# Optimization experiments

Hardware: AMD Instinct MI355X
Metric: run time of the kernel (lower is better)

Reference implementation:

```python
import jax, jax.numpy as jnp
import numpy as np

B, S_ENC, S_DEC, ENC_H, DEC_H = 8, 2048, 2048, 512, 512


def setup_inputs() -> dict:
    key = jax.random.key(0)
    k1, k2, k3 = jax.random.split(key, 3)
    return {
        "enc_hidden_states": jax.random.normal(k1, (B, S_ENC, ENC_H), dtype=jnp.float32),
        "dec_hidden_states": jax.random.normal(k2, (B, S_DEC, DEC_H), dtype=jnp.float32),
        "W_att": jax.random.normal(k3, (ENC_H, DEC_H), dtype=jnp.float32),
    }


def reference(enc_hidden_states, dec_hidden_states, W_att):
    # Project encoder states: [B, S_enc, dec_h]
    enc_proj = jnp.einsum("bse,ed->bsd", enc_hidden_states, W_att)
    # Luong 'general' scores for all decoder timesteps at once: [B, S_dec, S_enc]
    # (original code loops over decoder timesteps via tf.map_fn; this is the
    # equivalent single batched matmul)
    att_logits = jnp.einsum("btd,bsd->bts", dec_hidden_states, enc_proj)
    att_softmax = jax.nn.softmax(att_logits, axis=-1)
    # Attention context vectors: [B, S_dec, enc_h]
    att_vector = jnp.einsum("bts,bse->bte", att_softmax, enc_hidden_states)
    return att_vector
```

## Files before the change

kernel.cpp:

```cpp
#include <hip/hip_runtime.h>
#include <cstdint>


#define DEVINL __device__ __forceinline__

typedef __attribute__((ext_vector_type(8))) short short8;
typedef __attribute__((ext_vector_type(4))) float f32x4;

DEVINL short f2bf(float x) {
    union { float f; uint32_t u; } v; v.f = x;
    uint32_t r = v.u + 0x7FFFu + ((v.u >> 16) & 1u);
    return (short)(r >> 16);
}
DEVINL float bf2f(short h) {
    union { uint32_t u; float f; } v; v.u = ((uint32_t)(uint16_t)h) << 16;
    return v.f;
}

DEVINL void gload_lds16(const void* g, void* l) {
    __builtin_amdgcn_global_load_lds(
        (const __attribute__((address_space(1))) char*)g,
        (__attribute__((address_space(3))) char*)l, 16, 0, 0);
}

__global__ __launch_bounds__(256)
void split_kernel(const float* __restrict__ x, short* __restrict__ hi,
                  short* __restrict__ lo)
{
    long i = ((long)blockIdx.x * 256 + threadIdx.x) * 8;
    f32x4 a = *(const f32x4*)(x + i);
    f32x4 b = *(const f32x4*)(x + i + 4);
    short8 h, l;
#pragma unroll
    for (int j = 0; j < 4; j++) {
        short ha = f2bf(a[j]); h[j] = ha;     l[j] = f2bf(a[j] - bf2f(ha));
        short hb = f2bf(b[j]); h[4 + j] = hb; l[4 + j] = f2bf(b[j] - bf2f(hb));
    }
    *(short8*)(hi + i) = h;
    *(short8*)(lo + i) = l;
}

__global__ __launch_bounds__(256)
void split_w_kernel(const float* __restrict__ w, short* __restrict__ wth,
                    short* __restrict__ wtl)
{
    int idx = blockIdx.x * 256 + threadIdx.x;
    int k = idx >> 9, n = idx & 511;
    float v = w[idx];
    short h = f2bf(v);
    wth[(long)n * 512 + k] = h;
    wtl[(long)n * 512 + k] = f2bf(v - bf2f(h));
}

__global__ __launch_bounds__(256)
void transpose_bf16_kernel(const float* __restrict__ x, short* __restrict__ xt)
{
    __shared__ short tile[32][33];
    const int b  = blockIdx.z;
    const int s0 = blockIdx.x * 32;
    const int e0 = blockIdx.y * 32;
    const float* px = x + (long)b * 2048 * 512;
    short* pt = xt + (long)b * 512 * 2048;
    const int tx = threadIdx.x & 31;
    const int ty = threadIdx.x >> 5;
#pragma unroll
    for (int r = 0; r < 32; r += 8)
        tile[ty + r][tx] = f2bf(px[(long)(s0 + ty + r) * 512 + e0 + tx]);
    __syncthreads();
#pragma unroll
    for (int r = 0; r < 32; r += 8)
        pt[(long)(e0 + ty + r) * 2048 + s0 + tx] = tile[tx][ty + r];
}

template<int NTERMS, bool SPLIT_OUT>
__global__ __launch_bounds__(256, 2)
void gemm_bt(const short* __restrict__ Ah, const short* __restrict__ Al,
             const short* __restrict__ Bh, const short* __restrict__ Bl,
             float* __restrict__ C, short* __restrict__ Ch, short* __restrict__ Cl,
             int K, int lda, int ldb, int ldc,
             long sA, long sB, long sC)
{
    extern __shared__ char smem_raw[];
    constexpr int OPS = (NTERMS == 3) ? 4 : 2;
    constexpr int SET = 128 * 32 * OPS;
    short* smem = (short*)smem_raw;

    const int tid  = threadIdx.x;
    const int wave = tid >> 6;
    const int lane = tid & 63;
    const int quad = lane >> 4;
    const int l16  = lane & 15;
    const int wm   = (wave >> 1) * 64;
    const int wn   = (wave & 1) * 64;

    const long tile_m = (long)blockIdx.y * 128;
    const long tile_n = (long)blockIdx.x * 128;
    const int  bz     = blockIdx.z;

    const short* pAh = Ah + (long)bz * sA;
    const short* pBh = Bh + (long)bz * sB;
    const short* pAl = (NTERMS == 3) ? (Al + (long)bz * sA) : nullptr;
    const short* pBl = (NTERMS == 3) ? (Bl + (long)bz * sB) : nullptr;

    const int srow = tid >> 2;
    const int skq  = (tid & 3) * 8;
    const int lds_off = srow * 32 + skq;
    const long ga0 = (tile_m + srow) * (long)lda + skq;
    const long gb0 = (tile_n + srow) * (long)ldb + skq;

    auto stage = [&](int k0, int buf) {
        short* s   = smem + buf * SET;
        short* ash = s;
        short* bsh = s + 128 * 32;
        gload_lds16(pAh + ga0 + k0,             ash + lds_off);
        gload_lds16(pAh + ga0 + 64l * lda + k0, ash + lds_off + 64 * 32);
        gload_lds16(pBh + gb0 + k0,             bsh + lds_off);
        gload_lds16(pBh + gb0 + 64l * ldb + k0, bsh + lds_off + 64 * 32);
        if constexpr (NTERMS == 3) {
            short* asl = s + 2 * 128 * 32;
            short* bsl = s + 3 * 128 * 32;
            gload_lds16(pAl + ga0 + k0,             asl + lds_off);
            gload_lds16(pAl + ga0 + 64l * lda + k0, asl + lds_off + 64 * 32);
            gload_lds16(pBl + gb0 + k0,             bsl + lds_off);
            gload_lds16(pBl + gb0 + 64l * ldb + k0, bsl + lds_off + 64 * 32);
        }
    };

    f32x4 acc[4][4] = {};
    stage(0, 0);
    int cur = 0;

    for (int k0 = 0; k0 < K; k0 += 32) {
        __syncthreads();
        if (k0 + 32 < K) stage(k0 + 32, cur ^ 1);

        short* s   = smem + cur * SET;
        short* ash = s;
        short* bsh = s + 128 * 32;
        short* asl = s + 2 * 128 * 32;
        short* bsl = s + 3 * 128 * 32;

        short8 ah[4], bh[4], al[4], bl[4];
#pragma unroll
        for (int i = 0; i < 4; i++) {
            ah[i] = *(const short8*)&ash[(wm + i * 16 + l16) * 32 + quad * 8];
            bh[i] = *(const short8*)&bsh[(wn + i * 16 + l16) * 32 + quad * 8];
            if constexpr (NTERMS == 3) {
                al[i] = *(const short8*)&asl[(wm + i * 16 + l16) * 32 + quad * 8];
                bl[i] = *(const short8*)&bsl[(wn + i * 16 + l16) * 32 + quad * 8];
            }
        }
#pragma unroll
        for (int i = 0; i < 4; i++)
#pragma unroll
            for (int j = 0; j < 4; j++) {
                acc[i][j] = __builtin_amdgcn_mfma_f32_16x16x32_bf16(ah[i], bh[j], acc[i][j], 0, 0, 0);
                if constexpr (NTERMS == 3) {
                    acc[i][j] = __builtin_amdgcn_mfma_f32_16x16x32_bf16(ah[i], bl[j], acc[i][j], 0, 0, 0);
                    acc[i][j] = __builtin_amdgcn_mfma_f32_16x16x32_bf16(al[i], bh[j], acc[i][j], 0, 0, 0);
                }
            }
        cur ^= 1;
    }

#pragma unroll
    for (int i = 0; i < 4; i++)
#pragma unroll
        for (int j = 0; j < 4; j++) {
            const long row0 = tile_m + wm + i * 16 + quad * 4;
            const long col  = tile_n + wn + j * 16 + l16;
#pragma unroll
            for (int r = 0; r < 4; r++) {
                float v = acc[i][j][r];
                if constexpr (SPLIT_OUT) {
                    long idx = (long)bz * sC + (row0 + r) * (long)ldc + col;
                    short h = f2bf(v);
                    Ch[idx] = h;
                    Cl[idx] = f2bf(v - bf2f(h));
                } else {
                    C[(long)bz * sC + (row0 + r) * (long)ldc + col] = v;
                }
            }
        }
}

__global__ __launch_bounds__(512, 2)
void gemm3_256(const short* __restrict__ Ah, const short* __restrict__ Al,
               const short* __restrict__ Bh, const short* __restrict__ Bl,
               float* __restrict__ C,
               int K, int lda, int ldb, int ldc,
               long sA, long sB, long sC, int nbx, int nby)
{
    extern __shared__ char smem_raw[];
    short* smem = (short*)smem_raw;
    constexpr int PL  = 256 * 32;
    constexpr int SET = 4 * PL;

    const int t    = threadIdx.x;
    const int wave = t >> 6;
    const int lane = t & 63;
    const int quad = lane >> 4;
    const int l16  = lane & 15;
    const int wm   = (wave >> 2) * 128;
    const int wn   = (wave & 3) * 64;
    const int kslot8 = ((quad ^ ((l16 >> 1) & 3)) << 3);

    const int nwg = gridDim.x;
    const int wg  = blockIdx.x;
    const int swz = (wg & 7) * (nwg >> 3) + (wg >> 3);
    const int per_b = nbx * nby;
    const int bz  = swz / per_b;
    const int rem = swz - bz * per_b;
    const long tile_m = (long)(rem / nbx) * 256;
    const long tile_n = (long)(rem % nbx) * 256;

    const short* pAh = Ah + (long)bz * sA;
    const short* pAl = Al + (long)bz * sA;
    const short* pBh = Bh + (long)bz * sB;
    const short* pBl = Bl + (long)bz * sB;

    const int srow   = t >> 2;
    const int schunk = (t & 3) ^ ((t >> 3) & 3);
    const long gA  = (tile_m + srow) * (long)lda + schunk * 8;
    const long gB  = (tile_n + srow) * (long)ldb + schunk * 8;
    const long gA2 = gA + 128l * lda;
    const long gB2 = gB + 128l * ldb;
    const int ld0 = t * 8;

    auto stage = [&](int k0, int buf) {
        short* s = smem + buf * SET;
        gload_lds16(pAh + gA  + k0, s + ld0);
        gload_lds16(pAh + gA2 + k0, s + ld0 + 4096);
        gload_lds16(pAl + gA  + k0, s + PL + ld0);
        gload_lds16(pAl + gA2 + k0, s + PL + ld0 + 4096);
        gload_lds16(pBh + gB  + k0, s + 2 * PL + ld0);
        gload_lds16(pBh + gB2 + k0, s + 2 * PL + ld0 + 4096);
        gload_lds16(pBl + gB  + k0, s + 3 * PL + ld0);
        gload_lds16(pBl + gB2 + k0, s + 3 * PL + ld0 + 4096);
    };

    f32x4 acc[8][4] = {};
    stage(0, 0);
    int cur = 0;

    for (int k0 = 0; k0 < K; k0 += 32) {
        if (k0 + 32 < K) {
            stage(k0 + 32, cur ^ 1);
            asm volatile("s_waitcnt vmcnt(8)" ::: "memory");
        } else {
            asm volatile("s_waitcnt vmcnt(0)" ::: "memory");
        }
        __builtin_amdgcn_s_barrier();

        const short* s    = smem + cur * SET;
        const short* ah_p = s;
        const short* al_p = s + PL;
        const short* bh_p = s + 2 * PL;
        const short* bl_p = s + 3 * PL;

        short8 bh[4], bl[4], ah[4], al[4];
#pragma unroll
        for (int j = 0; j < 4; j++) {
            bh[j] = *(const short8*)&bh_p[(wn + j * 16 + l16) * 32 + kslot8];
            bl[j] = *(const short8*)&bl_p[(wn + j * 16 + l16) * 32 + kslot8];
        }
#pragma unroll
        for (int i = 0; i < 4; i++) {
            ah[i] = *(const short8*)&ah_p[(wm + i * 16 + l16) * 32 + kslot8];
            al[i] = *(const short8*)&al_p[(wm + i * 16 + l16) * 32 + kslot8];
        }
        __builtin_amdgcn_s_setprio(1);
#pragma unroll
        for (int i = 0; i < 4; i++)
#pragma unroll
            for (int j = 0; j < 4; j++) {
                acc[i][j] = __builtin_amdgcn_mfma_f32_16x16x32_bf16(ah[i], bh[j], acc[i][j], 0, 0, 0);
                acc[i][j] = __builtin_amdgcn_mfma_f32_16x16x32_bf16(ah[i], bl[j], acc[i][j], 0, 0, 0);
                acc[i][j] = __builtin_amdgcn_mfma_f32_16x16x32_bf16(al[i], bh[j], acc[i][j], 0, 0, 0);
            }
        __builtin_amdgcn_s_setprio(0);
#pragma unroll
        for (int i = 0; i < 4; i++) {
            ah[i] = *(const short8*)&ah_p[(wm + 64 + i * 16 + l16) * 32 + kslot8];
            al[i] = *(const short8*)&al_p[(wm + 64 + i * 16 + l16) * 32 + kslot8];
        }
        __builtin_amdgcn_s_setprio(1);
#pragma unroll
        for (int i = 0; i < 4; i++)
#pragma unroll
            for (int j = 0; j < 4; j++) {
                acc[4 + i][j] = __builtin_amdgcn_mfma_f32_16x16x32_bf16(ah[i], bh[j], acc[4 + i][j], 0, 0, 0);
                acc[4 + i][j] = __builtin_amdgcn_mfma_f32_16x16x32_bf16(ah[i], bl[j], acc[4 + i][j], 0, 0, 0);
                acc[4 + i][j] = __builtin_amdgcn_mfma_f32_16x16x32_bf16(al[i], bh[j], acc[4 + i][j], 0, 0, 0);
            }
        __builtin_amdgcn_s_setprio(0);
        __builtin_amdgcn_s_barrier();
        cur ^= 1;
    }

#pragma unroll
    for (int i = 0; i < 8; i++)
#pragma unroll
        for (int j = 0; j < 4; j++) {
            const long row0 = tile_m + wm + i * 16 + quad * 4;
            const long col  = tile_n + wn + j * 16 + l16;
#pragma unroll
            for (int r = 0; r < 4; r++)
                C[(long)bz * sC + (row0 + r) * (long)ldc + col] = acc[i][j][r];
        }
}

__global__ __launch_bounds__(256)
void softmax_kernel(const float* __restrict__ logits, short* __restrict__ P)
{
    const long row = blockIdx.x;
    const float* p = logits + row * 2048;
    const int tid = threadIdx.x;
    const int lane = tid & 63, wave = tid >> 6;

    f32x4 v0 = *(const f32x4*)(p + tid * 8);
    f32x4 v1 = *(const f32x4*)(p + tid * 8 + 4);

    float m = fmaxf(fmaxf(fmaxf(v0[0], v0[1]), fmaxf(v0[2], v0[3])),
                    fmaxf(fmaxf(v1[0], v1[1]), fmaxf(v1[2], v1[3])));
#pragma unroll
    for (int o = 32; o > 0; o >>= 1) m = fmaxf(m, __shfl_xor(m, o));

    __shared__ float red[8];
    if (lane == 0) red[wave] = m;
    __syncthreads();
    m = fmaxf(fmaxf(red[0], red[1]), fmaxf(red[2], red[3]));

    float e[8];
    float s = 0.f;
#pragma unroll
    for (int i = 0; i < 4; i++) { e[i] = __expf(v0[i] - m); s += e[i]; }
#pragma unroll
    for (int i = 0; i < 4; i++) { e[4 + i] = __expf(v1[i] - m); s += e[4 + i]; }
#pragma unroll
    for (int o = 32; o > 0; o >>= 1) s += __shfl_xor(s, o);
    if (lane == 0) red[4 + wave] = s;
    __syncthreads();
    const float inv = 1.f / (red[4] + red[5] + red[6] + red[7]);

    short8 ob;
#pragma unroll
    for (int i = 0; i < 8; i++) ob[i] = f2bf(e[i] * inv);
    *(short8*)(P + row * 2048 + tid * 8) = ob;
}

extern "C" void kernel_launch(void* const* d_in, const int* in_sizes, int n_in,
                              void* d_out, int out_size, void* d_ws, size_t ws_size,
                              hipStream_t stream)
{
    const float* enc = (const float*)d_in[0];
    const float* dec = (const float*)d_in[1];
    const float* W   = (const float*)d_in[2];
    float* out = (float*)d_out;

    const long BSE = 8l * 2048 * 512;
    const long NW  = 512l * 512;

    char* p = (char*)d_ws;
    auto take = [&](long bytes) { char* r = p; p += (bytes + 255) & ~255l; return r; };
    short* enc_hi = (short*)take(BSE * 2);
    short* enc_lo = (short*)take(BSE * 2);
    short* dec_hi = (short*)take(BSE * 2);
    short* dec_lo = (short*)take(BSE * 2);
    short* ep_hi  = (short*)take(BSE * 2);
    short* ep_lo  = (short*)take(BSE * 2);
    short* enc_t  = (short*)take(BSE * 2);
    short* wt_hi  = (short*)take(NW * 2);
    short* wt_lo  = (short*)take(NW * 2);
    float* logits = (float*)take(8l * 2048 * 2048 * 4);
    short* Pbuf = enc_hi;
    (void)ws_size; (void)in_sizes; (void)n_in; (void)out_size;

    static bool attr_set = false;
    if (!attr_set) {
        (void)hipFuncSetAttribute((const void*)gemm3_256,
                                  hipFuncAttributeMaxDynamicSharedMemorySize,
                                  131072);
        attr_set = true;
    }

    split_kernel<<<4096, 256, 0, stream>>>(enc, enc_hi, enc_lo);
    split_kernel<<<4096, 256, 0, stream>>>(dec, dec_hi, dec_lo);
    split_w_kernel<<<1024, 256, 0, stream>>>(W, wt_hi, wt_lo);
    transpose_bf16_kernel<<<dim3(64, 16, 8), 256, 0, stream>>>(enc, enc_t);

    gemm_bt<3, true><<<dim3(4, 128, 1), 256, 64 * 1024, stream>>>(
        enc_hi, enc_lo, wt_hi, wt_lo, nullptr, ep_hi, ep_lo,
        512, 512, 512, 512, 0, 0, 0);

    gemm3_256<<<512, 512, 131072, stream>>>(
        dec_hi, dec_lo, ep_hi, ep_lo, logits,
        512, 512, 512, 2048, 2048l * 512, 2048l * 512, 2048l * 2048, 8, 8);

    softmax_kernel<<<16384, 256, 0, stream>>>(logits, Pbuf);

    gemm_bt<1, false><<<dim3(4, 16, 8), 256, 32 * 1024, stream>>>(
        Pbuf, nullptr, enc_t, nullptr, out, nullptr, nullptr,
        2048, 2048, 2048, 512, 2048l * 2048, 512l * 2048, 2048l * 512);
}
```

Baseline: 350.0 us.

## Split split-bf16 GEMM k-step into three phased MFMA passes with staggered loads

Restructures the main loop of the split-precision (hi/lo bf16) GEMM. Each k-step now runs three passes (Ah*Bh, Al*Bh, Ah*Bl) over the full 8x4 accumulator tile instead of two halves each interleaving three MFMAs. The global-to-LDS prefetch of the next tile is split into per-plane chunks issued between passes, with finer vmcnt waits and extra barriers. The aim is to overlap the loads with MFMA work and cut the number of register fragments held live at once, at the cost of more barriers and reloading the Ah fragments from LDS.

```diff
diff --git a/kernel.cpp b/kernel.cpp
--- a/kernel.cpp
+++ b/kernel.cpp
@@ -227,74 +227,106 @@
     const long gB2 = gB + 128l * ldb;
     const int ld0 = t * 8;
 
-    auto stage = [&](int k0, int buf) {
-        short* s = smem + buf * SET;
-        gload_lds16(pAh + gA  + k0, s + ld0);
-        gload_lds16(pAh + gA2 + k0, s + ld0 + 4096);
-        gload_lds16(pAl + gA  + k0, s + PL + ld0);
-        gload_lds16(pAl + gA2 + k0, s + PL + ld0 + 4096);
-        gload_lds16(pBh + gB  + k0, s + 2 * PL + ld0);
-        gload_lds16(pBh + gB2 + k0, s + 2 * PL + ld0 + 4096);
-        gload_lds16(pBl + gB  + k0, s + 3 * PL + ld0);
-        gload_lds16(pBl + gB2 + k0, s + 3 * PL + ld0 + 4096);
-    };
-
     f32x4 acc[8][4] = {};
-    stage(0, 0);
+
+    {
+        short* s = smem;
+        gload_lds16(pAh + gA,  s + ld0);
+        gload_lds16(pAh + gA2, s + ld0 + 4096);
+        gload_lds16(pBh + gB,  s + 2 * PL + ld0);
+        gload_lds16(pBh + gB2, s + 2 * PL + ld0 + 4096);
+        gload_lds16(pAl + gA,  s + PL + ld0);
+        gload_lds16(pAl + gA2, s + PL + ld0 + 4096);
+        gload_lds16(pBl + gB,  s + 3 * PL + ld0);
+        gload_lds16(pBl + gB2, s + 3 * PL + ld0 + 4096);
+    }
+    asm volatile("s_waitcnt vmcnt(4)" ::: "memory");
+    __builtin_amdgcn_s_barrier();
+
+    const int NT = K >> 5;
     int cur = 0;
-
-    for (int k0 = 0; k0 < K; k0 += 32) {
-        if (k0 + 32 < K) {
-            stage(k0 + 32, cur ^ 1);
-            asm volatile("s_waitcnt vmcnt(8)" ::: "memory");
-        } else {
-            asm volatile("s_waitcnt vmcnt(0)" ::: "memory");
-        }
-        __builtin_amdgcn_s_barrier();
-
-        const short* s    = smem + cur * SET;
+#pragma unroll 1
+    for (int kt = 0; kt < NT; ++kt) {
+        const short* s  = smem + cur * SET;
+        short* sn       = smem + (cur ^ 1) * SET;
         const short* ah_p = s;
         const short* al_p = s + PL;
         const short* bh_p = s + 2 * PL;
         const short* bl_p = s + 3 * PL;
-
-        short8 bh[4], bl[4], ah[4], al[4];
-#pragma unroll
-        for (int j = 0; j < 4; j++) {
-            bh[j] = *(const short8*)&bh_p[(wn + j * 16 + l16) * 32 + kslot8];
-            bl[j] = *(const short8*)&bl_p[(wn + j * 16 + l16) * 32 + kslot8];
-        }
-#pragma unroll
-        for (int i = 0; i < 4; i++) {
-            ah[i] = *(const short8*)&ah_p[(wm + i * 16 + l16) * 32 + kslot8];
-            al[i] = *(const short8*)&al_p[(wm + i * 16 + l16) * 32 + kslot8];
-        }
+        const int  k0n  = (kt + 1) << 5;
+        const bool more = (kt + 1 < NT);
+
+        short8 xa[8], xb[4];
+
+#pragma unroll
+        for (int i = 0; i < 8; i++)
+            xa[i] = *(const short8*)&ah_p[(wm + i * 16 + l16) * 32 + kslot8];
+#pragma unroll
+        for (int j = 0; j < 4; j++)
+            xb[j] = *(const short8*)&bh_p[(wn + j * 16 + l16) * 32 + kslot8];
+        if (more) {
+            gload_lds16(pAh + gA  + k0n, sn + ld0);
+            gload_lds16(pAh + gA2 + k0n, sn + ld0 + 4096);
+            gload_lds16(pBh + gB  + k0n, sn + 2 * PL + ld0);
+            gload_lds16(pBh + gB2 + k0n, sn + 2 * PL + ld0 + 4096);
+            asm volatile("s_waitcnt vmcnt(6)" ::: "memory");
+        } else {
+            asm volatile("s_waitcnt vmcnt(2)" ::: "memory");
+        }
+        __builtin_amdgcn_s_barrier();
+        asm volatile("s_waitcnt lgkmcnt(0)" ::: "memory");
         __builtin_amdgcn_s_setprio(1);
 #pragma unroll
-        for (int i = 0; i < 4; i++)
-#pragma unroll
-            for (int j = 0; j < 4; j++) {
-                acc[i][j] = __builtin_amdgcn_mfma_f32_16x16x32_bf16(ah[i], bh[j], acc[i][j], 0, 0, 0);
-                acc[i][j] = __builtin_amdgcn_mfma_f32_16x16x32_bf16(ah[i], bl[j], acc[i][j], 0, 0, 0);
-                acc[i][j] = __builtin_amdgcn_mfma_f32_16x16x32_bf16(al[i], bh[j], acc[i][j], 0, 0, 0);
-            }
+        for (int i = 0; i < 8; i++)
+#pragma unroll
+            for (int j = 0; j < 4; j++)
+                acc[i][j] = __builtin_amdgcn_mfma_f32_16x16x32_bf16(xa[i], xb[j], acc[i][j], 0, 0, 0);
         __builtin_amdgcn_s_setprio(0);
-#pragma unroll
-        for (int i = 0; i < 4; i++) {
-            ah[i] = *(const short8*)&ah_p[(wm + 64 + i * 16 + l16) * 32 + kslot8];
-            al[i] = *(const short8*)&al_p[(wm + 64 + i * 16 + l16) * 32 + kslot8];
-        }
+        __builtin_amdgcn_s_barrier();
+
+#pragma unroll
+        for (int i = 0; i < 8; i++)
+            xa[i] = *(const short8*)&al_p[(wm + i * 16 + l16) * 32 + kslot8];
+        if (more) {
+            gload_lds16(pAl + gA  + k0n, sn + PL + ld0);
+            gload_lds16(pAl + gA2 + k0n, sn + PL + ld0 + 4096);
+            asm volatile("s_waitcnt vmcnt(6)" ::: "memory");
+        } else {
+            asm volatile("s_waitcnt vmcnt(0)" ::: "memory");
+        }
+        __builtin_amdgcn_s_barrier();
+        asm volatile("s_waitcnt lgkmcnt(0)" ::: "memory");
         __builtin_amdgcn_s_setprio(1);
 #pragma unroll
-        for (int i = 0; i < 4; i++)
-#pragma unroll
-            for (int j = 0; j < 4; j++) {
-                acc[4 + i][j] = __builtin_amdgcn_mfma_f32_16x16x32_bf16(ah[i], bh[j], acc[4 + i][j], 0, 0, 0);
-                acc[4 + i][j] = __builtin_amdgcn_mfma_f32_16x16x32_bf16(ah[i], bl[j], acc[4 + i][j], 0, 0, 0);
-                acc[4 + i][j] = __builtin_amdgcn_mfma_f32_16x16x32_bf16(al[i], bh[j], acc[4 + i][j], 0, 0, 0);
-            }
+        for (int i = 0; i < 8; i++)
+#pragma unroll
+            for (int j = 0; j < 4; j++)
+                acc[i][j] = __builtin_amdgcn_mfma_f32_16x16x32_bf16(xa[i], xb[j], acc[i][j], 0, 0, 0);
         __builtin_amdgcn_s_setprio(0);
         __builtin_amdgcn_s_barrier();
+
+#pragma unroll
+        for (int j = 0; j < 4; j++)
+            xb[j] = *(const short8*)&bl_p[(wn + j * 16 + l16) * 32 + kslot8];
+#pragma unroll
+        for (int i = 0; i < 8; i++)
+            xa[i] = *(const short8*)&ah_p[(wm + i * 16 + l16) * 32 + kslot8];
+        if (more) {
+            gload_lds16(pBl + gB  + k0n, sn + 3 * PL + ld0);
+            gload_lds16(pBl + gB2 + k0n, sn + 3 * PL + ld0 + 4096);
+            asm volatile("s_waitcnt vmcnt(4)" ::: "memory");
+        }
+        __builtin_amdgcn_s_barrier();
+        asm volatile("s_waitcnt lgkmcnt(0)" ::: "memory");
+        __builtin_amdgcn_s_setprio(1);
+#pragma unroll
+        for (int i = 0; i < 8; i++)
+#pragma unroll
+            for (int j = 0; j < 4; j++)
+                acc[i][j] = __builtin_amdgcn_mfma_f32_16x16x32_bf16(xa[i], xb[j], acc[i][j], 0, 0, 0);
+        __builtin_amdgcn_s_setprio(0);
+        __builtin_amdgcn_s_barrier();
+
         cur ^= 1;
     }
 
```

New measurement: 346.2 us. Within noise of the previous version (-1.1%).
